# Kernel optimization log

Hardware: AMD Instinct MI355X
Metric: run time of the kernel (lower is better)

Reference implementation:

```python
import jax, jax.numpy as jnp
import numpy as np
import math

ETA = 0.01
SIG = 5.0


def _conv2d(x, w, b, pad):
    # x: (B, Cin, H, W), w: (Cout, Cin, kh, kw)
    y = jax.lax.conv_general_dilated(
        x, w, window_strides=(1, 1), padding=[(pad, pad), (pad, pad)],
        dimension_numbers=('NCHW', 'OIHW', 'NCHW'))
    return y + b[None, :, None, None]


def _sim_flow(x, corr_w, corr_b):
    # x: (N, C, T, H, W)
    N, C, T, H, W = x.shape
    Tp = T - 1
    # correspond_conv: ReLU -> 1x1x1 Conv3d (C -> C//2)
    tm = jnp.einsum('oc,ncthw->nothw', corr_w, jax.nn.relu(x)) + corr_b[None, :, None, None, None]
    tm = tm.transpose(0, 2, 1, 3, 4)  # (N, T, C//2, H, W)
    bh = tm[:, 1:]   # (N, Tp, Cp, H, W)
    bf = tm[:, :-1]
    # full correlation volume: (N, Tp, H, W, H, W); (a,b)=bh coords, (u,v)=bf coords
    score = jnp.einsum('ntcab,ntcuv->ntabuv', bh, bf)
    flat = score.reshape(N, Tp, H * W, H, W)
    max_score = flat.max(axis=2, keepdims=True)             # (N, Tp, 1, H, W)
    inds = jnp.argmax(flat, axis=2)[:, :, None]             # (N, Tp, 1, H, W)
    idx_x = (inds // H).astype(score.dtype)                 # faithful: // H as in source
    idx_y = (inds % H).astype(score.dtype)
    px = jnp.arange(H, dtype=score.dtype).reshape(1, 1, H, 1, 1)
    py = jnp.arange(W, dtype=score.dtype).reshape(1, 1, W, 1, 1)
    norm = math.sqrt(2.0 * math.pi) * SIG
    g_x = jnp.exp((px - idx_x) / (SIG ** 2)) / norm         # (N, Tp, H, H, W)
    g_y = jnp.exp((py - idx_y) / (SIG ** 2)) / norm         # (N, Tp, W, H, W)
    score_x = (g_x[:, :, :, None, :, :] * score).reshape(N, Tp, H * W, H, W)
    coef_x = jax.nn.softmax(score_x / ETA, axis=2)
    score_y = (g_y[:, :, None, :, :, :] * score).reshape(N, Tp, H * W, H, W)
    coef_y = jax.nn.softmax(score_y / ETA, axis=2)
    epx = jnp.repeat(jnp.arange(H, dtype=score.dtype), W).reshape(1, 1, H * W, 1, 1)
    epy = jnp.tile(jnp.arange(W, dtype=score.dtype), H).reshape(1, 1, H * W, 1, 1)
    d_x = (epx * coef_x).sum(axis=2, keepdims=True)         # (N, Tp, 1, H, W)
    d_y = (epy * coef_y).sum(axis=2, keepdims=True)
    return jnp.concatenate([d_x, d_y, max_score], axis=2)   # (N, Tp, 3, H, W)


def setup_inputs() -> dict:
    key = jax.random.key(0)
    ks = jax.random.split(key, 8)
    N, C, T, H, W = 4, 256, 8, 28, 28
    Cp = C // 2
    s = 0.05
    return {
        'input_tem_map': jax.random.normal(ks[0], (N, C, T, H, W), jnp.float32),
        'corr_w': jax.random.normal(ks[1], (Cp, C), jnp.float32) * s,
        'corr_b': jnp.zeros((Cp,), jnp.float32),
        'mw1': jax.random.normal(ks[2], (64, 3, 5, 5), jnp.float32) * s,
        'mb1': jnp.zeros((64,), jnp.float32),
        'mw2': jax.random.normal(ks[3], (128, 64, 3, 3), jnp.float32) * s,
        'mb2': jnp.zeros((128,), jnp.float32),
        'mw3': jax.random.normal(ks[4], (Cp, 128, 3, 3), jnp.float32) * s,
        'mb3': jnp.zeros((Cp,), jnp.float32),
        'mw4': jax.random.normal(ks[5], (C, Cp, 3, 3), jnp.float32) * s,
        'mb4': jnp.zeros((C,), jnp.float32),
        'lin_w': jax.random.normal(ks[6], (C, C), jnp.float32) * s,
        'lin_b': jnp.zeros((C,), jnp.float32),
    }


def reference(input_tem_map, corr_w, corr_b, mw1, mb1, mw2, mb2, mw3, mb3, mw4, mb4, lin_w, lin_b):
    x = input_tem_map
    N, C, T, H, W = x.shape
    Tp = T - 1
    y = x.mean(axis=(2, 3, 4))                               # appearance vector (N, C)
    sim = _sim_flow(x, corr_w, corr_b)                       # (N, Tp, 3, H, W)
    # motion_conv: all time kernels are 1 -> fold Tp into batch and use 2D convs
    m = jax.nn.relu(sim).reshape(N * Tp, 3, H, W)
    m = jax.nn.relu(_conv2d(m, mw1, mb1, 1))                 # k5 pad1 -> (H-2, W-2)
    m = jax.nn.relu(_conv2d(m, mw2, mb2, 1))
    m = jax.nn.relu(_conv2d(m, mw3, mb3, 1))
    m = _conv2d(m, mw4, mb4, 1)                              # (N*Tp, C, H-2, W-2)
    motion_vec = m.reshape(N, Tp, C, H - 2, W - 2).mean(axis=(1, 3, 4))  # (N, C)
    z = jax.nn.relu(y + motion_vec) @ lin_w.T + lin_b        # W = ReLU -> Linear
    return z
```

## Files before the change

kernel.cpp:

```cpp
#include <hip/hip_runtime.h>


#define NORM_INV 0.07978845608028654f

typedef __attribute__((ext_vector_type(8))) short bf16x8;
typedef __attribute__((ext_vector_type(4))) float f32x4;

__device__ inline ushort f2bf(float v) {
  union { float f; uint u; } c; c.f = v;
  const uint u = c.u + 0x7FFFu + ((c.u >> 16) & 1u);
  return (ushort)(u >> 16);
}
__device__ inline float bf2f(ushort h) {
  union { uint u; float f; } c; c.u = ((uint)h) << 16;
  return c.f;
}

__global__ __launch_bounds__(256) void xb_kernel(const float* __restrict__ x,
    ushort* __restrict__ xh, ushort* __restrict__ xl) {
  const int tid = threadIdx.x;
  const int p0 = blockIdx.x * 64;
  const int c0 = blockIdx.y * 64;
  const int nt = blockIdx.z;
  const int n = nt >> 3, t = nt & 7;
  __shared__ float tile[64][65];
  const float* xp = x + (((size_t)n * 256 + c0) * 8 + t) * 784;
#pragma unroll
  for (int i = 0; i < 16; ++i) {
    const int idx = i * 256 + tid;
    const int c = idx >> 6, p = idx & 63;
    const int hw = p0 + p;
    tile[p][c] = (hw < 784) ? xp[(size_t)c * 6272 + hw] : 0.f;
  }
  __syncthreads();
#pragma unroll
  for (int i = 0; i < 8; ++i) {
    const int idx = i * 256 + tid;
    const int p = idx >> 5, c2 = (idx & 31) * 2;
    const int hw = p0 + p;
    if (hw < 784) {
      const size_t o = ((size_t)nt * 784 + hw) * 256 + c0 + c2;
      const float v0 = fmaxf(tile[p][c2], 0.f);
      const float v1 = fmaxf(tile[p][c2 + 1], 0.f);
      const ushort h0 = f2bf(v0), h1 = f2bf(v1);
      ushort2 hv, lv;
      hv.x = h0; hv.y = h1;
      lv.x = f2bf(v0 - bf2f(h0)); lv.y = f2bf(v1 - bf2f(h1));
      *(ushort2*)(xh + o) = hv;
      *(ushort2*)(xl + o) = lv;
    }
  }
}

__global__ __launch_bounds__(256) void pack_cw_kernel(const float* __restrict__ cw,
    ushort* __restrict__ bh, ushort* __restrict__ bl) {
  const int idx = blockIdx.x * 256 + threadIdx.x;
  const int j = idx & 7, l = (idx >> 3) & 63, rest = idx >> 9;
  const int n16 = rest & 7, kc = rest >> 3;
  const int co = n16 * 16 + (l & 15);
  const int k = kc * 32 + (l >> 4) * 8 + j;
  const float v = cw[co * 256 + k];
  const ushort h = f2bf(v);
  bh[idx] = h;
  bl[idx] = f2bf(v - bf2f(h));
}

__global__ __launch_bounds__(256) void tm_gemm_kernel(
    const ushort* __restrict__ xh, const ushort* __restrict__ xl,
    const ushort* __restrict__ bph, const ushort* __restrict__ bpl,
    const float* __restrict__ cb, ushort* __restrict__ tmt) {
  const int tid = threadIdx.x;
  const int w = tid >> 6, l = tid & 63;
  const int lr = l & 15, lq = l >> 4;
  const int mtile = blockIdx.x * 4 + w;
  const int ntile = blockIdx.y;
  const size_t r0 = (size_t)(mtile * 32 + lr) * 256 + lq * 8;
  const size_t r1 = r0 + 16 * 256;
  f32x4 acc[2][2];
#pragma unroll
  for (int mf = 0; mf < 2; ++mf)
#pragma unroll
    for (int nf = 0; nf < 2; ++nf) { f32x4 z = {0.f,0.f,0.f,0.f}; acc[mf][nf] = z; }
#pragma unroll
  for (int kc = 0; kc < 8; ++kc) {
    const bf16x8 ah0 = *(const bf16x8*)(xh + r0 + kc * 32);
    const bf16x8 ah1 = *(const bf16x8*)(xh + r1 + kc * 32);
    const bf16x8 al0 = *(const bf16x8*)(xl + r0 + kc * 32);
    const bf16x8 al1 = *(const bf16x8*)(xl + r1 + kc * 32);
    const size_t bo = ((size_t)(kc * 8 + ntile * 2) * 64 + l) * 8;
    const bf16x8 bh0 = *(const bf16x8*)(bph + bo);
    const bf16x8 bh1 = *(const bf16x8*)(bph + bo + 512);
    const bf16x8 bl0 = *(const bf16x8*)(bpl + bo);
    const bf16x8 bl1 = *(const bf16x8*)(bpl + bo + 512);
    acc[0][0] = __builtin_amdgcn_mfma_f32_16x16x32_bf16(ah0, bh0, acc[0][0], 0,0,0);
    acc[0][1] = __builtin_amdgcn_mfma_f32_16x16x32_bf16(ah0, bh1, acc[0][1], 0,0,0);
    acc[1][0] = __builtin_amdgcn_mfma_f32_16x16x32_bf16(ah1, bh0, acc[1][0], 0,0,0);
    acc[1][1] = __builtin_amdgcn_mfma_f32_16x16x32_bf16(ah1, bh1, acc[1][1], 0,0,0);
    acc[0][0] = __builtin_amdgcn_mfma_f32_16x16x32_bf16(al0, bh0, acc[0][0], 0,0,0);
    acc[0][1] = __builtin_amdgcn_mfma_f32_16x16x32_bf16(al0, bh1, acc[0][1], 0,0,0);
    acc[1][0] = __builtin_amdgcn_mfma_f32_16x16x32_bf16(al1, bh0, acc[1][0], 0,0,0);
    acc[1][1] = __builtin_amdgcn_mfma_f32_16x16x32_bf16(al1, bh1, acc[1][1], 0,0,0);
    acc[0][0] = __builtin_amdgcn_mfma_f32_16x16x32_bf16(ah0, bl0, acc[0][0], 0,0,0);
    acc[0][1] = __builtin_amdgcn_mfma_f32_16x16x32_bf16(ah0, bl1, acc[0][1], 0,0,0);
    acc[1][0] = __builtin_amdgcn_mfma_f32_16x16x32_bf16(ah1, bl0, acc[1][0], 0,0,0);
    acc[1][1] = __builtin_amdgcn_mfma_f32_16x16x32_bf16(ah1, bl1, acc[1][1], 0,0,0);
  }
#pragma unroll
  for (int nf = 0; nf < 2; ++nf) {
    const int co = ntile * 32 + nf * 16 + lr;
    const float bv = cb[co];
#pragma unroll
    for (int mf = 0; mf < 2; ++mf)
#pragma unroll
      for (int r = 0; r < 4; ++r) {
        const int pix = mtile * 32 + mf * 16 + lq * 4 + r;
        tmt[(size_t)pix * 128 + co] = f2bf(acc[mf][nf][r] + bv);
      }
  }
}

__global__ __launch_bounds__(512) void score_kernel(const ushort* __restrict__ tmt,
    float* __restrict__ m0) {
  const int tid = threadIdx.x;
  const int nt = blockIdx.y;
  const int n = nt / 7, t = nt % 7;
  const int uv0 = blockIdx.x * 16;
  const ushort* bfp = tmt + (size_t)(n * 8 + t) * 784 * 128;
  const ushort* bhp = tmt + (size_t)(n * 8 + t + 1) * 784 * 128;
  __shared__ float sc[16 * 785];
  __shared__ float gt[16 * 64];
  const int w = tid >> 6;
  const int l = tid & 63;
  const int lr = l & 15, lq = l >> 4;
  bf16x8 af[4];
#pragma unroll
  for (int kc = 0; kc < 4; ++kc)
    af[kc] = *(const bf16x8*)(bfp + (uv0 + lr) * 128 + kc * 32 + lq * 8);
  f32x4 acc[7];
#pragma unroll
  for (int i = 0; i < 7; ++i) { f32x4 z = {0.f,0.f,0.f,0.f}; acc[i] = z; }
#pragma unroll
  for (int i = 0; i < 7; ++i) {
    const int nf = i * 8 + w;
    if (nf < 49) {
      const ushort* bp = bhp + (nf * 16 + lr) * 128 + lq * 8;
      const bf16x8 b0 = *(const bf16x8*)(bp);
      const bf16x8 b1 = *(const bf16x8*)(bp + 32);
      const bf16x8 b2 = *(const bf16x8*)(bp + 64);
      const bf16x8 b3 = *(const bf16x8*)(bp + 96);
      acc[i] = __builtin_amdgcn_mfma_f32_16x16x32_bf16(af[0], b0, acc[i], 0,0,0);
      acc[i] = __builtin_amdgcn_mfma_f32_16x16x32_bf16(af[1], b1, acc[i], 0,0,0);
      acc[i] = __builtin_amdgcn_mfma_f32_16x16x32_bf16(af[2], b2, acc[i], 0,0,0);
      acc[i] = __builtin_amdgcn_mfma_f32_16x16x32_bf16(af[3], b3, acc[i], 0,0,0);
    }
  }
#pragma unroll
  for (int i = 0; i < 7; ++i) {
    const int nf = i * 8 + w;
    if (nf < 49) {
#pragma unroll
      for (int r = 0; r < 4; ++r)
        sc[(lq * 4 + r) * 785 + nf * 16 + lr] = acc[i][r];
    }
  }
  __syncthreads();
  const int row = tid >> 5, l32 = tid & 31;
  const float* rowp = &sc[row * 785];
  float bv = -1e30f; int bi = 0;
#pragma unroll 5
  for (int i = 0; i < 25; ++i) {
    const int a2 = i * 32 + l32;
    if (a2 < 784) {
      const float v = rowp[a2];
      if (v > bv) { bv = v; bi = a2; }
    }
  }
#pragma unroll
  for (int off = 16; off; off >>= 1) {
    const float ov = __shfl_xor(bv, off, 32);
    const int oi = __shfl_xor(bi, off, 32);
    if (ov > bv || (ov == bv && oi < bi)) { bv = ov; bi = oi; }
  }
  const int ast = bi / 28;
  const int bst = bi - ast * 28;
  float* g = &gt[row * 64];
  if (l32 < 28) {
    g[l32]      = __expf((float)(l32 - ast) * 0.04f) * NORM_INV;
    g[32 + l32] = __expf((float)(l32 - bst) * 0.04f) * NORM_INV;
  }
  float mx = -1e30f, my = -1e30f;
#pragma unroll 5
  for (int i = 0; i < 25; ++i) {
    const int a2 = i * 32 + l32;
    if (a2 < 784) {
      const float v = rowp[a2];
      const int a = a2 / 28; const int bb = a2 - a * 28;
      mx = fmaxf(mx, g[a] * v); my = fmaxf(my, g[32 + bb] * v);
    }
  }
#pragma unroll
  for (int off = 16; off; off >>= 1) {
    mx = fmaxf(mx, __shfl_xor(mx, off, 32));
    my = fmaxf(my, __shfl_xor(my, off, 32));
  }
  float sx = 0.f, sxw = 0.f, sy = 0.f, syw = 0.f;
#pragma unroll 5
  for (int i = 0; i < 25; ++i) {
    const int a2 = i * 32 + l32;
    if (a2 < 784) {
      const float v = rowp[a2];
      const int a = a2 / 28; const int bb = a2 - a * 28;
      const float ex = __expf((g[a] * v - mx) * 100.f);
      const float ey = __expf((g[32 + bb] * v - my) * 100.f);
      sx += ex; sxw += (float)a * ex;
      sy += ey; syw += (float)bb * ey;
    }
  }
#pragma unroll
  for (int off = 16; off; off >>= 1) {
    sx += __shfl_xor(sx, off, 32); sxw += __shfl_xor(sxw, off, 32);
    sy += __shfl_xor(sy, off, 32); syw += __shfl_xor(syw, off, 32);
  }
  if (l32 == 0) {
    const int uv = uv0 + row;
    float* op = m0 + (size_t)nt * 3 * 784 + uv;
    op[0]    = fmaxf(sxw / sx, 0.f);
    op[784]  = fmaxf(syw / sy, 0.f);
    op[1568] = fmaxf(bv, 0.f);
  }
}

__global__ __launch_bounds__(256) void conv1_kernel(const float* __restrict__ m0,
    const float* __restrict__ w, const float* __restrict__ bias,
    ushort* __restrict__ out) {
  const int b = blockIdx.z;
  const int pg = blockIdx.y;
  const int co0 = blockIdx.x * 16;
  const int tid = threadIdx.x;
  __shared__ float il[3 * 784];
  __shared__ float wl[75 * 16];
  const float* ip = m0 + (size_t)b * 2352;
  for (int i = tid; i < 2352; i += 256) il[i] = ip[i];
  for (int i = tid; i < 1200; i += 256) {
    const int c = i & 15, rest = i >> 4;
    wl[i] = w[(size_t)(co0 + c) * 75 + rest];
  }
  __syncthreads();
  const int pix = pg * 256 + tid;
  if (pix >= 676) return;
  const int py = pix / 26, px = pix - py * 26;
  float acc[16];
#pragma unroll
  for (int c = 0; c < 16; ++c) acc[c] = 0.f;
  for (int ci = 0; ci < 3; ++ci) {
#pragma unroll
    for (int dy = 0; dy < 5; ++dy) {
      const int iy = py + dy - 1;
      if ((unsigned)iy >= 28u) continue;
#pragma unroll
      for (int dx = 0; dx < 5; ++dx) {
        const int ix = px + dx - 1;
        if ((unsigned)ix >= 28u) continue;
        const float v = il[ci * 784 + iy * 28 + ix];
        const float* wp = &wl[(ci * 25 + dy * 5 + dx) * 16];
#pragma unroll
        for (int c4 = 0; c4 < 16; c4 += 4) {
          const float4 wv = *(const float4*)&wp[c4];
          acc[c4 + 0] += wv.x * v; acc[c4 + 1] += wv.y * v;
          acc[c4 + 2] += wv.z * v; acc[c4 + 3] += wv.w * v;
        }
      }
    }
  }
  const int ipo = (py + 1) * 28 + px + 1;
  ushort* op = out + ((size_t)b * 784 + ipo) * 64 + co0;
#pragma unroll
  for (int c = 0; c < 16; ++c)
    op[c] = f2bf(fmaxf(acc[c] + bias[co0 + c], 0.f));
}

__global__ __launch_bounds__(256) void pack_w_kernel(const float* __restrict__ w,
    ushort* __restrict__ Bp, int CIN, int N16, int total) {
  const int idx = blockIdx.x * 256 + threadIdx.x;
  if (idx >= total) return;
  const int j = idx & 7;
  const int l = (idx >> 3) & 63;
  const int rest = idx >> 9;
  const int n16 = rest % N16;
  const int kc = rest / N16;
  const int co = n16 * 16 + (l & 15);
  const int kk = kc * 32 + (l >> 4) * 8 + j;
  const int tap = kk / CIN;
  const int ci = kk - tap * CIN;
  Bp[idx] = f2bf(w[((size_t)co * CIN + ci) * 9 + tap]);
}

template<int CIN, bool FINAL>
__global__ __launch_bounds__(256) void conv_mfma2_kernel(
    const ushort* __restrict__ in, const ushort* __restrict__ Bp,
    const float* __restrict__ bias, ushort* __restrict__ outp,
    float* __restrict__ outf, int COUTC) {
  constexpr int KC = CIN * 9 / 32;
  constexpr int CPG = CIN / 32;
  const int N16 = COUTC >> 4;
  const int tid = threadIdx.x;
  const int w = tid >> 6, l = tid & 63;
  const int lr = l & 15, lq = l >> 4;
  const int mtile = blockIdx.x * 4 + w;
  const int ntile = blockIdx.y;
  const ushort* aP[2];
#pragma unroll
  for (int mf = 0; mf < 2; ++mf) {
    int P = mtile * 32 + mf * 16 + lr;
    if (P > 18927) P = 18927;
    const int b = P / 676;
    const int pp = P - b * 676;
    const int ipb = pp + 2 * (pp / 26);
    aP[mf] = in + ((size_t)b * 784 + ipb) * CIN;
  }
  f32x4 acc[2][2];
#pragma unroll
  for (int mf = 0; mf < 2; ++mf)
#pragma unroll
    for (int nf = 0; nf < 2; ++nf) { f32x4 z = {0.f,0.f,0.f,0.f}; acc[mf][nf] = z; }

  auto loadA = [&](int kc, bf16x8* a) {
    const int tap = kc / CPG;
    const int ci0 = (kc - tap * CPG) * 32 + lq * 8;
    const int off = (tap / 3) * 28 + (tap - (tap / 3) * 3);
    a[0] = *(const bf16x8*)(aP[0] + (size_t)off * CIN + ci0);
    a[1] = *(const bf16x8*)(aP[1] + (size_t)off * CIN + ci0);
  };
  auto loadB = [&](int kc, bf16x8* bb) {
    const ushort* bp = Bp + (((size_t)kc * N16 + ntile * 2) * 64 + l) * 8;
    bb[0] = *(const bf16x8*)bp;
    bb[1] = *(const bf16x8*)(bp + 512);
  };
  auto domfma = [&](bf16x8* a, bf16x8* bb) {
    acc[0][0] = __builtin_amdgcn_mfma_f32_16x16x32_bf16(a[0], bb[0], acc[0][0], 0,0,0);
    acc[0][1] = __builtin_amdgcn_mfma_f32_16x16x32_bf16(a[0], bb[1], acc[0][1], 0,0,0);
    acc[1][0] = __builtin_amdgcn_mfma_f32_16x16x32_bf16(a[1], bb[0], acc[1][0], 0,0,0);
    acc[1][1] = __builtin_amdgcn_mfma_f32_16x16x32_bf16(a[1], bb[1], acc[1][1], 0,0,0);
  };

  bf16x8 aA[2], bA[2], aB[2], bB[2];
  loadA(0, aA); loadB(0, bA);
  for (int kc = 0; kc < KC; kc += 2) {
    loadA(kc + 1, aB); loadB(kc + 1, bB);
    domfma(aA, bA);
    if (kc + 2 < KC) { loadA(kc + 2, aA); loadB(kc + 2, bA); }
    domfma(aB, bB);
  }
#pragma unroll
  for (int nf = 0; nf < 2; ++nf) {
    const int co = ntile * 32 + nf * 16 + lr;
    const float bvv = bias[co];
#pragma unroll
    for (int mf = 0; mf < 2; ++mf) {
#pragma unroll
      for (int r = 0; r < 4; ++r) {
        const int P = mtile * 32 + mf * 16 + lq * 4 + r;
        if (P < 18928) {
          const int b = P / 676;
          const int pp = P - b * 676;
          const float v = acc[mf][nf][r] + bvv;
          if constexpr (FINAL) {
            outf[((size_t)b * COUTC + co) * 676 + pp] = v;
          } else {
            const int ipo = pp + 2 * (pp / 26) + 29;
            outp[((size_t)b * 784 + ipo) * COUTC + co] = f2bf(fmaxf(v, 0.f));
          }
        }
      }
    }
  }
}

__global__ __launch_bounds__(256) void final_reduce_kernel(const float* __restrict__ x,
    const float* __restrict__ m4, float* __restrict__ r) {
  const int nc = blockIdx.x;
  const int n = nc >> 8, c = nc & 255;
  const int tid = threadIdx.x;
  const float* xs = x + (size_t)nc * 6272;
  float s = 0.f;
  for (int i = tid; i < 6272; i += 256) s += xs[i];
  float s2 = 0.f;
  for (int t = 0; t < 7; ++t) {
    const float* ms = m4 + ((size_t)(n * 7 + t) * 256 + c) * 676;
    for (int i = tid; i < 676; i += 256) s2 += ms[i];
  }
  float v = s * (1.f / 6272.f) + s2 * (1.f / 4732.f);
#pragma unroll
  for (int off = 32; off; off >>= 1) v += __shfl_down(v, off);
  __shared__ float red[4];
  if ((tid & 63) == 0) red[tid >> 6] = v;
  __syncthreads();
  if (tid == 0) r[nc] = fmaxf(red[0] + red[1] + red[2] + red[3], 0.f);
}

__global__ __launch_bounds__(256) void linear_kernel(const float* __restrict__ r,
    const float* __restrict__ lw, const float* __restrict__ lb,
    float* __restrict__ out) {
  const int n = blockIdx.x;
  const int j = threadIdx.x;
  __shared__ float rl[256];
  rl[j] = r[n * 256 + j];
  __syncthreads();
  float acc = lb[j];
  const float* w = lw + (size_t)j * 256;
#pragma unroll 4
  for (int c = 0; c < 256; c += 4) {
    const float4 wv = *(const float4*)&w[c];
    acc += wv.x * rl[c] + wv.y * rl[c + 1] + wv.z * rl[c + 2] + wv.w * rl[c + 3];
  }
  out[n * 256 + j] = acc;
}

extern "C" void kernel_launch(void* const* d_in, const int* in_sizes, int n_in,
                              void* d_out, int out_size, void* d_ws, size_t ws_size,
                              hipStream_t stream) {
  const float* x      = (const float*)d_in[0];
  const float* corr_w = (const float*)d_in[1];
  const float* corr_b = (const float*)d_in[2];
  const float* mw1 = (const float*)d_in[3];
  const float* mb1 = (const float*)d_in[4];
  const float* mw2 = (const float*)d_in[5];
  const float* mb2 = (const float*)d_in[6];
  const float* mw3 = (const float*)d_in[7];
  const float* mb3 = (const float*)d_in[8];
  const float* mw4 = (const float*)d_in[9];
  const float* mb4 = (const float*)d_in[10];
  const float* lin_w = (const float*)d_in[11];
  const float* lin_b = (const float*)d_in[12];
  float* out = (float*)d_out;
  char* wsb = (char*)d_ws;

  ushort* xh  = (ushort*)(wsb + 0);
  ushort* xl  = (ushort*)(wsb + 12845056);
  ushort* tmt = (ushort*)(wsb + 25690112);
  float*  m4  = (float*)(wsb + 0);
  ushort* m1  = (ushort*)(wsb + 19382272);
  ushort* m2  = (ushort*)(wsb + 22192128);
  ushort* m3  = (ushort*)(wsb + 27811840);
  float*  m0  = (float*)(wsb + 33431552);
  float*  rr  = (float*)(wsb + 33694976);
  ushort* Bp2 = (ushort*)(wsb + 33699072);
  ushort* Bp3 = (ushort*)(wsb + 33846528);
  ushort* Bp4 = (ushort*)(wsb + 34141440);
  ushort* Bph = (ushort*)(wsb + 34731264);
  ushort* Bpl = (ushort*)(wsb + 34796800);

  pack_cw_kernel<<<dim3(128), 256, 0, stream>>>(corr_w, Bph, Bpl);
  pack_w_kernel<<<dim3(288), 256, 0, stream>>>(mw2, Bp2, 64, 8, 73728);
  pack_w_kernel<<<dim3(576), 256, 0, stream>>>(mw3, Bp3, 128, 8, 147456);
  pack_w_kernel<<<dim3(1152), 256, 0, stream>>>(mw4, Bp4, 128, 16, 294912);

  xb_kernel<<<dim3(13, 4, 32), 256, 0, stream>>>(x, xh, xl);
  tm_gemm_kernel<<<dim3(196, 4), 256, 0, stream>>>(xh, xl, Bph, Bpl, corr_b, tmt);
  score_kernel<<<dim3(49, 28), 512, 0, stream>>>(tmt, m0);

  hipMemsetAsync(m1, 0, 2809856, stream);
  hipMemsetAsync(m2, 0, 5619712, stream);
  hipMemsetAsync(m3, 0, 5619712, stream);

  conv1_kernel<<<dim3(4, 3, 28), 256, 0, stream>>>(m0, mw1, mb1, m1);
  conv_mfma2_kernel<64, false><<<dim3(148, 4), 256, 0, stream>>>(
      m1, Bp2, mb2, m2, nullptr, 128);
  conv_mfma2_kernel<128, false><<<dim3(148, 4), 256, 0, stream>>>(
      m2, Bp3, mb3, m3, nullptr, 128);
  conv_mfma2_kernel<128, true><<<dim3(148, 8), 256, 0, stream>>>(
      m3, Bp4, mb4, nullptr, m4, 256);
  final_reduce_kernel<<<dim3(1024), 256, 0, stream>>>(x, m4, rr);
  linear_kernel<<<dim3(4), 256, 0, stream>>>(rr, lin_w, lin_b, out);
}
```

Baseline: 341.2 us.

## Stage conv tiles through LDS, fuse weight packing, compute mean in xb

The three 3x3 MFMA convolutions now stage larger A and B tiles into double-buffered LDS with global_load_lds, so each wave reuses fragments across a 4-wide N block instead of reading global memory directly. The four weight-packing kernels merge into one launch, and the three full memsets become a kernel that zeroes only the padding border. The xb transpose kernel now uses float4 loads and accumulates the input mean with atomics, so final_reduce no longer re-reads x. Several unrelated launch-overhead and bandwidth ideas land together, and the atomic float sum makes the mean order-dependent.

```diff
diff --git a/kernel.cpp b/kernel.cpp
--- a/kernel.cpp
+++ b/kernel.cpp
@@ -16,8 +16,56 @@
   return c.f;
 }
 
+__device__ __forceinline__ void glds16(const void* g, void* l) {
+  __builtin_amdgcn_global_load_lds(
+      (const __attribute__((address_space(1))) void*)g,
+      (__attribute__((address_space(3))) void*)l, 16, 0, 0);
+}
+
+__device__ __forceinline__ void pack_w_one(const float* __restrict__ w,
+    ushort* __restrict__ Bp, int CIN, int N16, int idx) {
+  const int j = idx & 7;
+  const int l = (idx >> 3) & 63;
+  const int rest = idx >> 9;
+  const int n16 = rest % N16;
+  const int kc = rest / N16;
+  const int co = n16 * 16 + (l & 15);
+  const int kk = kc * 32 + (l >> 4) * 8 + j;
+  const int tap = kk / CIN;
+  const int ci = kk - tap * CIN;
+  Bp[idx] = f2bf(w[((size_t)co * CIN + ci) * 9 + tap]);
+}
+
+__global__ __launch_bounds__(256) void pack_all_kernel(
+    const float* __restrict__ cw, const float* __restrict__ mw2,
+    const float* __restrict__ mw3, const float* __restrict__ mw4,
+    ushort* __restrict__ bph, ushort* __restrict__ bpl,
+    ushort* __restrict__ bp2, ushort* __restrict__ bp3,
+    ushort* __restrict__ bp4, float* __restrict__ y) {
+  int idx = blockIdx.x * 256 + threadIdx.x;
+  if (idx < 32768) {
+    const int j = idx & 7, l = (idx >> 3) & 63, rest = idx >> 9;
+    const int n16 = rest & 7, kc = rest >> 3;
+    const int co = n16 * 16 + (l & 15);
+    const int k = kc * 32 + (l >> 4) * 8 + j;
+    const float v = cw[co * 256 + k];
+    const ushort h = f2bf(v);
+    bph[idx] = h;
+    bpl[idx] = f2bf(v - bf2f(h));
+    return;
+  }
+  idx -= 32768;
+  if (idx < 73728)  { pack_w_one(mw2, bp2, 64, 8, idx);  return; }
+  idx -= 73728;
+  if (idx < 147456) { pack_w_one(mw3, bp3, 128, 8, idx); return; }
+  idx -= 147456;
+  if (idx < 294912) { pack_w_one(mw4, bp4, 128, 16, idx); return; }
+  idx -= 294912;
+  if (idx < 1024) y[idx] = 0.f;
+}
+
 __global__ __launch_bounds__(256) void xb_kernel(const float* __restrict__ x,
-    ushort* __restrict__ xh, ushort* __restrict__ xl) {
+    ushort* __restrict__ xh, ushort* __restrict__ xl, float* __restrict__ y) {
   const int tid = threadIdx.x;
   const int p0 = blockIdx.x * 64;
   const int c0 = blockIdx.y * 64;
@@ -26,11 +74,20 @@
   __shared__ float tile[64][65];
   const float* xp = x + (((size_t)n * 256 + c0) * 8 + t) * 784;
 #pragma unroll
-  for (int i = 0; i < 16; ++i) {
+  for (int i = 0; i < 4; ++i) {
     const int idx = i * 256 + tid;
-    const int c = idx >> 6, p = idx & 63;
-    const int hw = p0 + p;
-    tile[p][c] = (hw < 784) ? xp[(size_t)c * 6272 + hw] : 0.f;
+    const int c = idx >> 4, q = idx & 15;
+    const int hw = p0 + q * 4;
+    const float* sp = xp + (size_t)c * 6272 + hw;
+    if (hw + 3 < 784) {
+      const float4 v = *(const float4*)sp;
+      tile[q * 4 + 0][c] = v.x; tile[q * 4 + 1][c] = v.y;
+      tile[q * 4 + 2][c] = v.z; tile[q * 4 + 3][c] = v.w;
+    } else {
+#pragma unroll
+      for (int e = 0; e < 4; ++e)
+        tile[q * 4 + e][c] = (hw + e < 784) ? sp[e] : 0.f;
+    }
   }
   __syncthreads();
 #pragma unroll
@@ -50,19 +107,12 @@
       *(ushort2*)(xl + o) = lv;
     }
   }
-}
-
-__global__ __launch_bounds__(256) void pack_cw_kernel(const float* __restrict__ cw,
-    ushort* __restrict__ bh, ushort* __restrict__ bl) {
-  const int idx = blockIdx.x * 256 + threadIdx.x;
-  const int j = idx & 7, l = (idx >> 3) & 63, rest = idx >> 9;
-  const int n16 = rest & 7, kc = rest >> 3;
-  const int co = n16 * 16 + (l & 15);
-  const int k = kc * 32 + (l >> 4) * 8 + j;
-  const float v = cw[co * 256 + k];
-  const ushort h = f2bf(v);
-  bh[idx] = h;
-  bl[idx] = f2bf(v - bf2f(h));
+  if (tid < 64) {
+    float s = 0.f;
+#pragma unroll 8
+    for (int p = 0; p < 64; ++p) s += tile[p][tid];
+    atomicAdd(y + n * 256 + c0 + tid, s);
+  }
 }
 
 __global__ __launch_bounds__(256) void tm_gemm_kernel(
@@ -230,6 +280,27 @@
   }
 }
 
+__global__ __launch_bounds__(256) void border_zero_kernel(
+    ushort* __restrict__ m1, ushort* __restrict__ m2, ushort* __restrict__ m3) {
+  const int idx = blockIdx.x * 256 + threadIdx.x;
+  if (idx >= 28 * 108 * 40) return;
+  const int c = idx % 40;
+  const int rest = idx / 40;
+  const int bp = rest % 108;
+  const int b = rest / 108;
+  int ipo;
+  if (bp < 28) ipo = bp;
+  else if (bp < 56) ipo = 756 + (bp - 28);
+  else {
+    const int r = 1 + (bp - 56) / 2;
+    ipo = r * 28 + ((bp - 56) & 1) * 27;
+  }
+  const bf16x8 z = {0,0,0,0,0,0,0,0};
+  if (c < 8)       *(bf16x8*)(m1 + ((size_t)b * 784 + ipo) * 64  + c * 8) = z;
+  else if (c < 24) *(bf16x8*)(m2 + ((size_t)b * 784 + ipo) * 128 + (c - 8) * 8) = z;
+  else             *(bf16x8*)(m3 + ((size_t)b * 784 + ipo) * 128 + (c - 24) * 8) = z;
+}
+
 __global__ __launch_bounds__(256) void conv1_kernel(const float* __restrict__ m0,
     const float* __restrict__ w, const float* __restrict__ bias,
     ushort* __restrict__ out) {
@@ -279,96 +350,99 @@
     op[c] = f2bf(fmaxf(acc[c] + bias[co0 + c], 0.f));
 }
 
-__global__ __launch_bounds__(256) void pack_w_kernel(const float* __restrict__ w,
-    ushort* __restrict__ Bp, int CIN, int N16, int total) {
-  const int idx = blockIdx.x * 256 + threadIdx.x;
-  if (idx >= total) return;
-  const int j = idx & 7;
-  const int l = (idx >> 3) & 63;
-  const int rest = idx >> 9;
-  const int n16 = rest % N16;
-  const int kc = rest / N16;
-  const int co = n16 * 16 + (l & 15);
-  const int kk = kc * 32 + (l >> 4) * 8 + j;
-  const int tap = kk / CIN;
-  const int ci = kk - tap * CIN;
-  Bp[idx] = f2bf(w[((size_t)co * CIN + ci) * 9 + tap]);
-}
-
-template<int CIN, bool FINAL>
-__global__ __launch_bounds__(256) void conv_mfma2_kernel(
+template<int CIN, int COUT, int BM, bool FINAL>
+__global__ __launch_bounds__(256) void conv_lds_kernel(
     const ushort* __restrict__ in, const ushort* __restrict__ Bp,
     const float* __restrict__ bias, ushort* __restrict__ outp,
-    float* __restrict__ outf, int COUTC) {
+    float* __restrict__ outf) {
   constexpr int KC = CIN * 9 / 32;
   constexpr int CPG = CIN / 32;
-  const int N16 = COUTC >> 4;
+  constexpr int N16 = COUT / 16;
+  constexpr int MF = BM / 32;
+  constexpr int PA = BM / 64;
+  constexpr int ABYTES = BM * 64;
+  __shared__ __align__(16) char lds[2 * ABYTES + 16384];
   const int tid = threadIdx.x;
   const int w = tid >> 6, l = tid & 63;
+  const int wm = w >> 1, wn = w & 1;
   const int lr = l & 15, lq = l >> 4;
-  const int mtile = blockIdx.x * 4 + w;
-  const int ntile = blockIdx.y;
-  const ushort* aP[2];
-#pragma unroll
-  for (int mf = 0; mf < 2; ++mf) {
-    int P = mtile * 32 + mf * 16 + lr;
-    if (P > 18927) P = 18927;
-    const int b = P / 676;
-    const int pp = P - b * 676;
+  const int mt = blockIdx.x, nt = blockIdx.y;
+
+  size_t srcA[PA];
+#pragma unroll
+  for (int p = 0; p < PA; ++p) {
+    const int e = p * 256 + tid;
+    const int P = e % BM, kq = e / BM;
+    int GP = mt * BM + P;
+    if (GP > 18927) GP = 18927;
+    const int b = GP / 676, pp = GP - b * 676;
     const int ipb = pp + 2 * (pp / 26);
-    aP[mf] = in + ((size_t)b * 784 + ipb) * CIN;
-  }
-  f32x4 acc[2][2];
-#pragma unroll
-  for (int mf = 0; mf < 2; ++mf)
-#pragma unroll
-    for (int nf = 0; nf < 2; ++nf) { f32x4 z = {0.f,0.f,0.f,0.f}; acc[mf][nf] = z; }
-
-  auto loadA = [&](int kc, bf16x8* a) {
+    srcA[p] = ((size_t)b * 784 + ipb) * CIN + kq * 8;
+  }
+
+  auto stage = [&](int kc, int buf) {
     const int tap = kc / CPG;
-    const int ci0 = (kc - tap * CPG) * 32 + lq * 8;
-    const int off = (tap / 3) * 28 + (tap - (tap / 3) * 3);
-    a[0] = *(const bf16x8*)(aP[0] + (size_t)off * CIN + ci0);
-    a[1] = *(const bf16x8*)(aP[1] + (size_t)off * CIN + ci0);
+    const int ktoff = ((tap / 3) * 28 + (tap - (tap / 3) * 3)) * CIN +
+                      (kc - tap * CPG) * 32;
+#pragma unroll
+    for (int p = 0; p < PA; ++p)
+      glds16(in + srcA[p] + ktoff,
+             lds + buf * ABYTES + p * 4096 + w * 1024);
+    const ushort* bsrc = Bp + ((size_t)kc * N16 + nt * 8) * 512;
+#pragma unroll
+    for (int p = 0; p < 2; ++p)
+      glds16(bsrc + p * 2048 + tid * 8,
+             lds + 2 * ABYTES + buf * 8192 + p * 4096 + w * 1024);
   };
-  auto loadB = [&](int kc, bf16x8* bb) {
-    const ushort* bp = Bp + (((size_t)kc * N16 + ntile * 2) * 64 + l) * 8;
-    bb[0] = *(const bf16x8*)bp;
-    bb[1] = *(const bf16x8*)(bp + 512);
-  };
-  auto domfma = [&](bf16x8* a, bf16x8* bb) {
-    acc[0][0] = __builtin_amdgcn_mfma_f32_16x16x32_bf16(a[0], bb[0], acc[0][0], 0,0,0);
-    acc[0][1] = __builtin_amdgcn_mfma_f32_16x16x32_bf16(a[0], bb[1], acc[0][1], 0,0,0);
-    acc[1][0] = __builtin_amdgcn_mfma_f32_16x16x32_bf16(a[1], bb[0], acc[1][0], 0,0,0);
-    acc[1][1] = __builtin_amdgcn_mfma_f32_16x16x32_bf16(a[1], bb[1], acc[1][1], 0,0,0);
-  };
-
-  bf16x8 aA[2], bA[2], aB[2], bB[2];
-  loadA(0, aA); loadB(0, bA);
-  for (int kc = 0; kc < KC; kc += 2) {
-    loadA(kc + 1, aB); loadB(kc + 1, bB);
-    domfma(aA, bA);
-    if (kc + 2 < KC) { loadA(kc + 2, aA); loadB(kc + 2, bA); }
-    domfma(aB, bB);
-  }
-#pragma unroll
-  for (int nf = 0; nf < 2; ++nf) {
-    const int co = ntile * 32 + nf * 16 + lr;
+
+  f32x4 acc[MF][4];
+#pragma unroll
+  for (int mf = 0; mf < MF; ++mf)
+#pragma unroll
+    for (int nf = 0; nf < 4; ++nf) { f32x4 z = {0.f,0.f,0.f,0.f}; acc[mf][nf] = z; }
+
+  stage(0, 0);
+  __syncthreads();
+  int buf = 0;
+  for (int kc = 0; kc < KC; ++kc) {
+    if (kc + 1 < KC) stage(kc + 1, buf ^ 1);
+    const char* Ab = lds + buf * ABYTES;
+    const char* Bb = lds + 2 * ABYTES + buf * 8192;
+    bf16x8 afr[MF], bfr[4];
+#pragma unroll
+    for (int mf = 0; mf < MF; ++mf)
+      afr[mf] = *(const bf16x8*)(Ab + lq * (BM * 16) +
+                                 (wm * (BM / 2) + mf * 16 + lr) * 16);
+#pragma unroll
+    for (int nf = 0; nf < 4; ++nf)
+      bfr[nf] = *(const bf16x8*)(Bb + ((wn * 4 + nf) * 64 + l) * 16);
+#pragma unroll
+    for (int mf = 0; mf < MF; ++mf)
+#pragma unroll
+      for (int nf = 0; nf < 4; ++nf)
+        acc[mf][nf] = __builtin_amdgcn_mfma_f32_16x16x32_bf16(
+            afr[mf], bfr[nf], acc[mf][nf], 0, 0, 0);
+    __syncthreads();
+    buf ^= 1;
+  }
+
+#pragma unroll
+  for (int nf = 0; nf < 4; ++nf) {
+    const int co = nt * 128 + wn * 64 + nf * 16 + lr;
     const float bvv = bias[co];
 #pragma unroll
-    for (int mf = 0; mf < 2; ++mf) {
+    for (int mf = 0; mf < MF; ++mf) {
 #pragma unroll
       for (int r = 0; r < 4; ++r) {
-        const int P = mtile * 32 + mf * 16 + lq * 4 + r;
+        const int P = mt * BM + wm * (BM / 2) + mf * 16 + lq * 4 + r;
         if (P < 18928) {
-          const int b = P / 676;
-          const int pp = P - b * 676;
+          const int b = P / 676, pp = P - b * 676;
           const float v = acc[mf][nf][r] + bvv;
           if constexpr (FINAL) {
-            outf[((size_t)b * COUTC + co) * 676 + pp] = v;
+            outf[((size_t)b * COUT + co) * 676 + pp] = v;
           } else {
             const int ipo = pp + 2 * (pp / 26) + 29;
-            outp[((size_t)b * 784 + ipo) * COUTC + co] = f2bf(fmaxf(v, 0.f));
+            outp[((size_t)b * 784 + ipo) * COUT + co] = f2bf(fmaxf(v, 0.f));
           }
         }
       }
@@ -376,26 +450,26 @@
   }
 }
 
-__global__ __launch_bounds__(256) void final_reduce_kernel(const float* __restrict__ x,
-    const float* __restrict__ m4, float* __restrict__ r) {
+__global__ __launch_bounds__(256) void final_reduce_kernel(
+    const float* __restrict__ y, const float* __restrict__ m4,
+    float* __restrict__ r) {
   const int nc = blockIdx.x;
   const int n = nc >> 8, c = nc & 255;
   const int tid = threadIdx.x;
-  const float* xs = x + (size_t)nc * 6272;
-  float s = 0.f;
-  for (int i = tid; i < 6272; i += 256) s += xs[i];
   float s2 = 0.f;
   for (int t = 0; t < 7; ++t) {
     const float* ms = m4 + ((size_t)(n * 7 + t) * 256 + c) * 676;
     for (int i = tid; i < 676; i += 256) s2 += ms[i];
   }
-  float v = s * (1.f / 6272.f) + s2 * (1.f / 4732.f);
-#pragma unroll
-  for (int off = 32; off; off >>= 1) v += __shfl_down(v, off);
+#pragma unroll
+  for (int off = 32; off; off >>= 1) s2 += __shfl_down(s2, off);
   __shared__ float red[4];
-  if ((tid & 63) == 0) red[tid >> 6] = v;
+  if ((tid & 63) == 0) red[tid >> 6] = s2;
   __syncthreads();
-  if (tid == 0) r[nc] = fmaxf(red[0] + red[1] + red[2] + red[3], 0.f);
+  if (tid == 0) {
+    const float tot = red[0] + red[1] + red[2] + red[3];
+    r[nc] = fmaxf(y[nc] * (1.f / 6272.f) + tot * (1.f / 4732.f), 0.f);
+  }
 }
 
 __global__ __launch_bounds__(256) void linear_kernel(const float* __restrict__ r,
@@ -449,27 +523,24 @@
   ushort* Bp4 = (ushort*)(wsb + 34141440);
   ushort* Bph = (ushort*)(wsb + 34731264);
   ushort* Bpl = (ushort*)(wsb + 34796800);
-
-  pack_cw_kernel<<<dim3(128), 256, 0, stream>>>(corr_w, Bph, Bpl);
-  pack_w_kernel<<<dim3(288), 256, 0, stream>>>(mw2, Bp2, 64, 8, 73728);
-  pack_w_kernel<<<dim3(576), 256, 0, stream>>>(mw3, Bp3, 128, 8, 147456);
-  pack_w_kernel<<<dim3(1152), 256, 0, stream>>>(mw4, Bp4, 128, 16, 294912);
-
-  xb_kernel<<<dim3(13, 4, 32), 256, 0, stream>>>(x, xh, xl);
+  float*  y   = (float*)(wsb + 34862336);
+
+  pack_all_kernel<<<dim3(2148), 256, 0, stream>>>(
+      corr_w, mw2, mw3, mw4, Bph, Bpl, Bp2, Bp3, Bp4, y);
+
+  xb_kernel<<<dim3(13, 4, 32), 256, 0, stream>>>(x, xh, xl, y);
   tm_gemm_kernel<<<dim3(196, 4), 256, 0, stream>>>(xh, xl, Bph, Bpl, corr_b, tmt);
   score_kernel<<<dim3(49, 28), 512, 0, stream>>>(tmt, m0);
 
-  hipMemsetAsync(m1, 0, 2809856, stream);
-  hipMemsetAsync(m2, 0, 5619712, stream);
-  hipMemsetAsync(m3, 0, 5619712, stream);
+  border_zero_kernel<<<dim3(473), 256, 0, stream>>>(m1, m2, m3);
 
   conv1_kernel<<<dim3(4, 3, 28), 256, 0, stream>>>(m0, mw1, mb1, m1);
-  conv_mfma2_kernel<64, false><<<dim3(148, 4), 256, 0, stream>>>(
-      m1, Bp2, mb2, m2, nullptr, 128);
-  conv_mfma2_kernel<128, false><<<dim3(148, 4), 256, 0, stream>>>(
-      m2, Bp3, mb3, m3, nullptr, 128);
-  conv_mfma2_kernel<128, true><<<dim3(148, 8), 256, 0, stream>>>(
-      m3, Bp4, mb4, nullptr, m4, 256);
-  final_reduce_kernel<<<dim3(1024), 256, 0, stream>>>(x, m4, rr);
+  conv_lds_kernel<64, 128, 64, false><<<dim3(296, 1), 256, 0, stream>>>(
+      m1, Bp2, mb2, m2, nullptr);
+  conv_lds_kernel<128, 128, 64, false><<<dim3(296, 1), 256, 0, stream>>>(
+      m2, Bp3, mb3, m3, nullptr);
+  conv_lds_kernel<128, 256, 128, true><<<dim3(148, 2), 256, 0, stream>>>(
+      m3, Bp4, mb4, nullptr, m4);
+  final_reduce_kernel<<<dim3(1024), 256, 0, stream>>>(y, m4, rr);
   linear_kernel<<<dim3(4), 256, 0, stream>>>(rr, lin_w, lin_b, out);
 }
```

Result: faster. 288.9 us (-15.3%).
